# Kernel tuning notes

Measured on AMD Instinct MI355X. Metric: run time of the kernel, lower is better.

## Reference

```python
import jax, jax.numpy as jnp
import numpy as np

D_MODEL = 1024
N_HEADS = 16
HEAD_DIM = D_MODEL // N_HEADS


def setup_inputs() -> dict:
    key = jax.random.key(0)
    k1, k2, k3 = jax.random.split(key, 3)
    B, T = 2, 2048
    x = jax.random.normal(k1, (B, T, D_MODEL), dtype=jnp.float32)
    # causal lower-triangular mask; positions with mask==0 are blocked
    mask = jnp.tril(jnp.ones((T, T), dtype=jnp.int32))
    s = 1.0 / np.sqrt(D_MODEL)
    W_qkv = jax.random.normal(k2, (D_MODEL, 3 * D_MODEL), dtype=jnp.float32) * s
    W_out = jax.random.normal(k3, (D_MODEL, D_MODEL), dtype=jnp.float32) * s
    return {"x": x, "mask": mask, "W_qkv": W_qkv, "W_out": W_out}


def reference(x, mask, W_qkv, W_out):
    B, T, C = x.shape
    qkv = x @ W_qkv  # [B, T, 3C]
    q, k, v = jnp.split(qkv, 3, axis=-1)
    # [B, H, T, Dh]
    def heads(t):
        return t.reshape(B, T, N_HEADS, HEAD_DIM).transpose(0, 2, 1, 3)
    q, k, v = heads(q), heads(k), heads(v)
    scale = jnp.float32(1.0 / np.sqrt(HEAD_DIM))
    attn = jnp.einsum("bhqd,bhkd->bhqk", q, k) * scale  # [B,H,T,T]
    attn = jnp.where(mask == 0, jnp.float32(-jnp.inf), attn)
    attn = jax.nn.softmax(attn, axis=-1)
    out = jnp.einsum("bhqk,bhkd->bhqd", attn, v)  # [B,H,T,Dh]
    out = out.transpose(0, 2, 1, 3).reshape(B, T, C)
    return out @ W_out
```

## Files before the change

### kernel.cpp

```cpp
#include <hip/hip_runtime.h>
#include <hip/hip_bf16.h>

typedef __bf16 bf16;
typedef __bf16 bf16x4 __attribute__((ext_vector_type(4)));
typedef __bf16 bf16x8 __attribute__((ext_vector_type(8)));
typedef float f32x4 __attribute__((ext_vector_type(4)));
typedef float f32x16 __attribute__((ext_vector_type(16)));
typedef unsigned int uint4v __attribute__((ext_vector_type(4)));

__device__ __forceinline__ void gld_lds16(const void* g, void* l) {
  __builtin_amdgcn_global_load_lds(
      (const __attribute__((address_space(1))) void*)g,
      (__attribute__((address_space(3))) void*)l, 16, 0, 0);
}

__device__ __forceinline__ unsigned pkbf(float a, float b) {
  union { bf16 h[2]; unsigned u; } x;
  x.h[0] = (bf16)a; x.h[1] = (bf16)b;
  return x.u;
}

__global__ __launch_bounds__(256) void cvt_kernel(const float* __restrict__ src,
                                                  bf16* __restrict__ dst, int n4) {
  int i = blockIdx.x * 256 + threadIdx.x;
  if (i < n4) {
    float4 v = ((const float4*)src)[i];
    bf16x4 o = { (bf16)v.x, (bf16)v.y, (bf16)v.z, (bf16)v.w };
    ((bf16x4*)dst)[i] = o;
  }
}

__global__ __launch_bounds__(256) void transpose_cvt_kernel(const float* __restrict__ src,
                                                            bf16* __restrict__ dst,
                                                            int R, int C) {
  __shared__ float tile[32][33];
  int tx = threadIdx.x & 31, ty = threadIdx.x >> 5;
  int bx = blockIdx.x * 32, by = blockIdx.y * 32;
#pragma unroll
  for (int j = 0; j < 32; j += 8)
    tile[ty + j][tx] = src[(size_t)(by + ty + j) * C + bx + tx];
  __syncthreads();
#pragma unroll
  for (int j = 0; j < 32; j += 8)
    dst[(size_t)(bx + ty + j) * R + by + tx] = (bf16)tile[tx][ty + j];
}

template <int MODE>
__global__ __launch_bounds__(256) void gemm_kernel(
    const bf16* __restrict__ A, const bf16* __restrict__ BT,
    float* __restrict__ Cf, bf16* __restrict__ qb, bf16* __restrict__ kb,
    bf16* __restrict__ vt, int M, int N, int K) {
  __shared__ bf16 As[128 * 32];
  __shared__ bf16 Bs[128 * 32];
  const int t = threadIdx.x;
  const int w = t >> 6, l = t & 63;
  const int bm = blockIdx.y * 128, bn = blockIdx.x * 128;
  const int wr = (w >> 1) * 64, wc = (w & 1) * 64;
  const int lr = l & 15, lh = l >> 4;
  f32x4 acc[4][4] = {};

  const bf16* Ab = A + (size_t)bm * K;
  const bf16* Bb = BT + (size_t)bn * K;
  const int srow = t >> 2;
  const int scol = (t & 3) * 8;
  char* AsB = (char*)As;
  char* BsB = (char*)Bs;
  const int ldsw = w * 1024;

  for (int k0 = 0; k0 < K; k0 += 32) {
    __syncthreads();
    gld_lds16(Ab + (size_t)srow * K + k0 + scol, AsB + ldsw);
    gld_lds16(Ab + (size_t)(srow + 64) * K + k0 + scol, AsB + 4096 + ldsw);
    gld_lds16(Bb + (size_t)srow * K + k0 + scol, BsB + ldsw);
    gld_lds16(Bb + (size_t)(srow + 64) * K + k0 + scol, BsB + 4096 + ldsw);
    __syncthreads();
    bf16x8 af[4], bfr[4];
#pragma unroll
    for (int m = 0; m < 4; ++m)
      af[m] = *(const bf16x8*)(AsB + (wr + m * 16 + lr) * 64 + lh * 16);
#pragma unroll
    for (int n = 0; n < 4; ++n)
      bfr[n] = *(const bf16x8*)(BsB + (wc + n * 16 + lr) * 64 + lh * 16);
#pragma unroll
    for (int m = 0; m < 4; ++m)
#pragma unroll
      for (int n = 0; n < 4; ++n)
        acc[m][n] = __builtin_amdgcn_mfma_f32_16x16x32_bf16(af[m], bfr[n],
                                                            acc[m][n], 0, 0, 0);
  }

  const int r0 = bm + wr + (lh << 2);
  const int c0 = bn + wc + lr;
#pragma unroll
  for (int m = 0; m < 4; ++m) {
#pragma unroll
    for (int n = 0; n < 4; ++n) {
#pragma unroll
      for (int r = 0; r < 4; ++r) {
        float v = acc[m][n][r];
        int row = r0 + m * 16 + r;
        int col = c0 + n * 16;
        if (MODE == 2) {
          Cf[(size_t)row * N + col] = v;
        } else {
          int bb = row >> 11, tt = row & 2047;
          if (col < 1024) {
            int h = col >> 6, d = col & 63;
            qb[(((size_t)(bb * 16 + h)) * 2048 + tt) * 64 + d] = (bf16)v;
          } else if (col < 2048) {
            int c = col - 1024, h = c >> 6, d = c & 63;
            kb[(((size_t)(bb * 16 + h)) * 2048 + tt) * 64 + d] = (bf16)v;
          } else {
            int c = col - 2048, h = c >> 6, d = c & 63;
            vt[(((size_t)(bb * 16 + h)) * 64 + d) * 2048 + tt] = (bf16)v;
          }
        }
      }
    }
  }
}

__global__ __launch_bounds__(256) void attn_kernel(const bf16* __restrict__ qb,
                                                   const bf16* __restrict__ kb,
                                                   const bf16* __restrict__ vt,
                                                   bf16* __restrict__ ao) {
  __shared__ bf16 plds[4][32][72];
  int wid = blockIdx.y * 16 + blockIdx.x;
  int swz = (wid & 7) * 64 + (wid >> 3);
  const int bh = swz >> 4;
  const int q0 = (swz & 15) * 128;
  const int w = threadIdx.x >> 6, l = threadIdx.x & 63;
  const int qw = q0 + w * 32;
  const int lq = l & 31, hi = l >> 5;
  const bf16* Qh = qb + (size_t)bh * 2048 * 64;
  const bf16* Kh = kb + (size_t)bh * 2048 * 64;
  const bf16* Vh = vt + (size_t)bh * 64 * 2048;

  bf16x8 qf[4];
#pragma unroll
  for (int c = 0; c < 4; ++c)
    qf[c] = *(const bf16x8*)(Qh + (size_t)(qw + lq) * 64 + c * 16 + hi * 8);

  f32x16 Ot0, Ot1;
#pragma unroll
  for (int r = 0; r < 16; ++r) { Ot0[r] = 0.f; Ot1[r] = 0.f; }
  float mrun = -1e30f, srun = 0.f;
  const int lastkt = qw >> 5;

  bf16x8 kA[4], vA[4], kB[4], vB[4];
#pragma unroll
  for (int c = 0; c < 4; ++c)
    kA[c] = *(const bf16x8*)(Kh + (size_t)lq * 64 + c * 16 + hi * 8);
#pragma unroll
  for (int df = 0; df < 2; ++df)
#pragma unroll
    for (int c = 0; c < 2; ++c)
      vA[df * 2 + c] = *(const bf16x8*)(Vh + (size_t)(df * 32 + lq) * 2048 + c * 16 + hi * 8);

  auto step = [&](bf16x8 (&KC)[4], bf16x8 (&VC)[4],
                  bf16x8 (&KN)[4], bf16x8 (&VN)[4], int kt) {
    const int kv0 = kt << 5;
    const int nkv0 = (kt < lastkt) ? kv0 + 32 : kv0;
#pragma unroll
    for (int c = 0; c < 4; ++c)
      KN[c] = *(const bf16x8*)(Kh + (size_t)(nkv0 + lq) * 64 + c * 16 + hi * 8);
#pragma unroll
    for (int df = 0; df < 2; ++df)
#pragma unroll
      for (int c = 0; c < 2; ++c)
        VN[df * 2 + c] = *(const bf16x8*)(Vh + (size_t)(df * 32 + lq) * 2048 + nkv0 + c * 16 + hi * 8);

    f32x16 S;
#pragma unroll
    for (int r = 0; r < 16; ++r) S[r] = 0.f;
#pragma unroll
    for (int c = 0; c < 4; ++c)
      S = __builtin_amdgcn_mfma_f32_32x32x16_bf16(KC[c], qf[c], S, 0, 0, 0);

    if (kt == lastkt) {
#pragma unroll
      for (int r = 0; r < 16; ++r) {
        int kvl = (r & 3) + 8 * (r >> 2) + 4 * hi;
        if (kvl > lq) S[r] = -1e30f;
      }
    }

    float mx[8];
#pragma unroll
    for (int i = 0; i < 8; ++i) mx[i] = fmaxf(S[2 * i], S[2 * i + 1]);
#pragma unroll
    for (int i = 0; i < 4; ++i) mx[i] = fmaxf(mx[i], mx[i + 4]);
    mx[0] = fmaxf(mx[0], mx[2]); mx[1] = fmaxf(mx[1], mx[3]);
    float smax = fmaxf(mx[0], mx[1]);
    float vmax = fmaxf(smax, __shfl_xor(smax, 32, 64));

    float mn = mrun;
    if (!__all(vmax <= mrun + 64.0f)) {
      mn = fmaxf(mrun, vmax);
      float al = __expf((mrun - mn) * 0.125f);
      srun *= al;
#pragma unroll
      for (int r = 0; r < 16; ++r) { Ot0[r] *= al; Ot1[r] *= al; }
      mrun = mn;
    }

    const float sc = 0.125f;
    const float nb = -mn * sc;
    float ps = 0.f;
    unsigned u_[8];
#pragma unroll
    for (int i = 0; i < 8; ++i) {
      float pa = __expf(fmaf(S[2 * i], sc, nb));
      float pb = __expf(fmaf(S[2 * i + 1], sc, nb));
      ps += pa + pb;
      u_[i] = pkbf(pa, pb);
    }
    ps += __shfl_xor(ps, 32, 64);
    srun += ps;

    unsigned s_[8];
#pragma unroll
    for (int i = 0; i < 8; ++i) s_[i] = __shfl_xor(u_[i], 32, 64);

    uint4v f0 = hi ? (uint4v){s_[2], s_[3], u_[2], u_[3]}
                   : (uint4v){u_[0], u_[1], s_[0], s_[1]};
    uint4v f1 = hi ? (uint4v){s_[6], s_[7], u_[6], u_[7]}
                   : (uint4v){u_[4], u_[5], s_[4], s_[5]};
    bf16x8 pf0 = __builtin_bit_cast(bf16x8, f0);
    bf16x8 pf1 = __builtin_bit_cast(bf16x8, f1);

    Ot0 = __builtin_amdgcn_mfma_f32_32x32x16_bf16(VC[0], pf0, Ot0, 0, 0, 0);
    Ot0 = __builtin_amdgcn_mfma_f32_32x32x16_bf16(VC[1], pf1, Ot0, 0, 0, 0);
    Ot1 = __builtin_amdgcn_mfma_f32_32x32x16_bf16(VC[2], pf0, Ot1, 0, 0, 0);
    Ot1 = __builtin_amdgcn_mfma_f32_32x32x16_bf16(VC[3], pf1, Ot1, 0, 0, 0);
  };

  for (int kt = 0; kt <= lastkt; ++kt) {
    if ((kt & 1) == 0) step(kA, vA, kB, vB, kt);
    else               step(kB, vB, kA, vA, kt);
  }

  float inv = 1.0f / srun;
#pragma unroll
  for (int r = 0; r < 16; r += 2) {
    int d0 = (r & 3) + 8 * (r >> 2) + 4 * hi;
    *(unsigned*)&plds[w][lq][d0]      = pkbf(Ot0[r] * inv, Ot0[r + 1] * inv);
    *(unsigned*)&plds[w][lq][32 + d0] = pkbf(Ot1[r] * inv, Ot1[r + 1] * inv);
  }
  __syncthreads();

  const int bb = bh >> 4, h = bh & 15;
  const int q = l >> 1, dh = (l & 1) * 32;
  size_t orow = ((size_t)(bb * 2048 + qw + q)) * 1024 + h * 64 + dh;
#pragma unroll
  for (int c = 0; c < 4; ++c) {
    bf16x8 vv = *(const bf16x8*)&plds[w][q][dh + c * 8];
    *(bf16x8*)(ao + orow + c * 8) = vv;
  }
}

extern "C" void kernel_launch(void* const* d_in, const int* in_sizes, int n_in,
                              void* d_out, int out_size, void* d_ws, size_t ws_size,
                              hipStream_t stream) {
  const float* x = (const float*)d_in[0];
  const float* Wqkv = (const float*)d_in[2];
  const float* Wout = (const float*)d_in[3];
  float* out = (float*)d_out;

  char* ws = (char*)d_ws;
  bf16* xb  = (bf16*)(ws);
  bf16* wqT = (bf16*)(ws + (size_t)(8 << 20));
  bf16* woT = (bf16*)(ws + (size_t)(14 << 20));
  bf16* qb  = (bf16*)(ws + (size_t)(16 << 20));
  bf16* kb  = (bf16*)(ws + (size_t)(24 << 20));
  bf16* vt  = (bf16*)(ws + (size_t)(32 << 20));
  bf16* ao  = (bf16*)(ws + (size_t)(40 << 20));

  cvt_kernel<<<dim3(4096), dim3(256), 0, stream>>>(x, xb, 1048576);
  transpose_cvt_kernel<<<dim3(96, 32), dim3(256), 0, stream>>>(Wqkv, wqT, 1024, 3072);
  transpose_cvt_kernel<<<dim3(32, 32), dim3(256), 0, stream>>>(Wout, woT, 1024, 1024);
  gemm_kernel<1><<<dim3(24, 32), dim3(256), 0, stream>>>(xb, wqT, nullptr, qb, kb, vt,
                                                         4096, 3072, 1024);
  attn_kernel<<<dim3(16, 32), dim3(256), 0, stream>>>(qb, kb, vt, ao);
  gemm_kernel<2><<<dim3(8, 32), dim3(256), 0, stream>>>(ao, woT, out, nullptr, nullptr,
                                                        nullptr, 4096, 1024, 1024);
}
```

Baseline: 273.7 us.

## Balance causal attention work by pairing query tiles and transpose V separately

Each attention wave now handles two 32-row query tiles, j and 63-j, so every wave does the same total number of causal KV steps. The grid stays the same size but each block does twice the tiles. The QKV GEMM now writes V in row layout and a new transpose kernel builds the transposed V, replacing the strided scatter stores in the GEMM epilogue. The softmax switches to exp2f with a pre-folded log2e scale, and the barrier before the per-wave LDS readback becomes a waitcnt. This adds one kernel launch and an extra pass over V in exchange for even load across waves and more coalesced GEMM stores.

New measurement: 307.5 us. 12.3% more time.

```diff
diff --git a/kernel.cpp b/kernel.cpp
--- a/kernel.cpp
+++ b/kernel.cpp
@@ -45,11 +45,29 @@
     dst[(size_t)(bx + ty + j) * R + by + tx] = (bf16)tile[tx][ty + j];
 }
 
+__global__ __launch_bounds__(256) void transpose_v_kernel(const bf16* __restrict__ src,
+                                                          bf16* __restrict__ dst) {
+  __shared__ bf16 tile[32][34];
+  int bh = blockIdx.z;
+  int t0 = blockIdx.x * 32;
+  int d0 = blockIdx.y * 32;
+  int tx = threadIdx.x & 31, ty = threadIdx.x >> 5;
+  const bf16* s = src + (size_t)bh * 2048 * 64;
+  bf16* d = dst + (size_t)bh * 64 * 2048;
+#pragma unroll
+  for (int j = 0; j < 32; j += 8)
+    tile[ty + j][tx] = s[(size_t)(t0 + ty + j) * 64 + d0 + tx];
+  __syncthreads();
+#pragma unroll
+  for (int j = 0; j < 32; j += 8)
+    d[(size_t)(d0 + ty + j) * 2048 + t0 + tx] = tile[tx][ty + j];
+}
+
 template <int MODE>
 __global__ __launch_bounds__(256) void gemm_kernel(
     const bf16* __restrict__ A, const bf16* __restrict__ BT,
     float* __restrict__ Cf, bf16* __restrict__ qb, bf16* __restrict__ kb,
-    bf16* __restrict__ vt, int M, int N, int K) {
+    bf16* __restrict__ vb, int M, int N, int K) {
   __shared__ bf16 As[128 * 32];
   __shared__ bf16 Bs[128 * 32];
   const int t = threadIdx.x;
@@ -112,7 +130,7 @@
             kb[(((size_t)(bb * 16 + h)) * 2048 + tt) * 64 + d] = (bf16)v;
           } else {
             int c = col - 2048, h = c >> 6, d = c & 63;
-            vt[(((size_t)(bb * 16 + h)) * 64 + d) * 2048 + tt] = (bf16)v;
+            vb[(((size_t)(bb * 16 + h)) * 2048 + tt) * 64 + d] = (bf16)v;
           }
         }
       }
@@ -128,134 +146,139 @@
   int wid = blockIdx.y * 16 + blockIdx.x;
   int swz = (wid & 7) * 64 + (wid >> 3);
   const int bh = swz >> 4;
-  const int q0 = (swz & 15) * 128;
+  const int grp = swz & 15;
   const int w = threadIdx.x >> 6, l = threadIdx.x & 63;
-  const int qw = q0 + w * 32;
+  const int jj = grp * 4 + w;
   const int lq = l & 31, hi = l >> 5;
   const bf16* Qh = qb + (size_t)bh * 2048 * 64;
   const bf16* Kh = kb + (size_t)bh * 2048 * 64;
   const bf16* Vh = vt + (size_t)bh * 64 * 2048;
-
-  bf16x8 qf[4];
-#pragma unroll
-  for (int c = 0; c < 4; ++c)
-    qf[c] = *(const bf16x8*)(Qh + (size_t)(qw + lq) * 64 + c * 16 + hi * 8);
-
-  f32x16 Ot0, Ot1;
-#pragma unroll
-  for (int r = 0; r < 16; ++r) { Ot0[r] = 0.f; Ot1[r] = 0.f; }
-  float mrun = -1e30f, srun = 0.f;
-  const int lastkt = qw >> 5;
-
-  bf16x8 kA[4], vA[4], kB[4], vB[4];
-#pragma unroll
-  for (int c = 0; c < 4; ++c)
-    kA[c] = *(const bf16x8*)(Kh + (size_t)lq * 64 + c * 16 + hi * 8);
-#pragma unroll
-  for (int df = 0; df < 2; ++df)
-#pragma unroll
-    for (int c = 0; c < 2; ++c)
-      vA[df * 2 + c] = *(const bf16x8*)(Vh + (size_t)(df * 32 + lq) * 2048 + c * 16 + hi * 8);
-
-  auto step = [&](bf16x8 (&KC)[4], bf16x8 (&VC)[4],
-                  bf16x8 (&KN)[4], bf16x8 (&VN)[4], int kt) {
-    const int kv0 = kt << 5;
-    const int nkv0 = (kt < lastkt) ? kv0 + 32 : kv0;
+  const int bb = bh >> 4, h = bh & 15;
+  const float sc2 = 0.125f * 1.4426950408889634f;
+
+#pragma unroll 1
+  for (int phase = 0; phase < 2; ++phase) {
+    const int qw = (phase ? (63 - jj) : jj) * 32;
+    const int lastkt = qw >> 5;
+
+    bf16x8 qf[4];
 #pragma unroll
     for (int c = 0; c < 4; ++c)
-      KN[c] = *(const bf16x8*)(Kh + (size_t)(nkv0 + lq) * 64 + c * 16 + hi * 8);
+      qf[c] = *(const bf16x8*)(Qh + (size_t)(qw + lq) * 64 + c * 16 + hi * 8);
+
+    f32x16 Ot0, Ot1;
+#pragma unroll
+    for (int r = 0; r < 16; ++r) { Ot0[r] = 0.f; Ot1[r] = 0.f; }
+    float mrun = -1e30f, srun = 0.f;
+
+    bf16x8 kA[4], vA[4], kB[4], vB[4];
+#pragma unroll
+    for (int c = 0; c < 4; ++c)
+      kA[c] = *(const bf16x8*)(Kh + (size_t)lq * 64 + c * 16 + hi * 8);
 #pragma unroll
     for (int df = 0; df < 2; ++df)
 #pragma unroll
       for (int c = 0; c < 2; ++c)
-        VN[df * 2 + c] = *(const bf16x8*)(Vh + (size_t)(df * 32 + lq) * 2048 + nkv0 + c * 16 + hi * 8);
-
-    f32x16 S;
-#pragma unroll
-    for (int r = 0; r < 16; ++r) S[r] = 0.f;
-#pragma unroll
-    for (int c = 0; c < 4; ++c)
-      S = __builtin_amdgcn_mfma_f32_32x32x16_bf16(KC[c], qf[c], S, 0, 0, 0);
-
-    if (kt == lastkt) {
-#pragma unroll
-      for (int r = 0; r < 16; ++r) {
-        int kvl = (r & 3) + 8 * (r >> 2) + 4 * hi;
-        if (kvl > lq) S[r] = -1e30f;
+        vA[df * 2 + c] = *(const bf16x8*)(Vh + (size_t)(df * 32 + lq) * 2048 + c * 16 + hi * 8);
+
+    auto step = [&](bf16x8 (&KC)[4], bf16x8 (&VC)[4],
+                    bf16x8 (&KN)[4], bf16x8 (&VN)[4], int kt) {
+      const int kv0 = kt << 5;
+      const int nkv0 = (kt < lastkt) ? kv0 + 32 : kv0;
+#pragma unroll
+      for (int c = 0; c < 4; ++c)
+        KN[c] = *(const bf16x8*)(Kh + (size_t)(nkv0 + lq) * 64 + c * 16 + hi * 8);
+#pragma unroll
+      for (int df = 0; df < 2; ++df)
+#pragma unroll
+        for (int c = 0; c < 2; ++c)
+          VN[df * 2 + c] = *(const bf16x8*)(Vh + (size_t)(df * 32 + lq) * 2048 + nkv0 + c * 16 + hi * 8);
+
+      f32x16 S;
+#pragma unroll
+      for (int r = 0; r < 16; ++r) S[r] = 0.f;
+#pragma unroll
+      for (int c = 0; c < 4; ++c)
+        S = __builtin_amdgcn_mfma_f32_32x32x16_bf16(KC[c], qf[c], S, 0, 0, 0);
+
+      if (kt == lastkt) {
+#pragma unroll
+        for (int r = 0; r < 16; ++r) {
+          int kvl = (r & 3) + 8 * (r >> 2) + 4 * hi;
+          if (kvl > lq) S[r] = -1e30f;
+        }
       }
+
+      float mx[8];
+#pragma unroll
+      for (int i = 0; i < 8; ++i) mx[i] = fmaxf(S[2 * i], S[2 * i + 1]);
+#pragma unroll
+      for (int i = 0; i < 4; ++i) mx[i] = fmaxf(mx[i], mx[i + 4]);
+      mx[0] = fmaxf(mx[0], mx[2]); mx[1] = fmaxf(mx[1], mx[3]);
+      float smax = fmaxf(mx[0], mx[1]);
+      float vmax = fmaxf(smax, __shfl_xor(smax, 32, 64));
+
+      float mn = mrun;
+      if (!__all(vmax <= mrun + 64.0f)) {
+        mn = fmaxf(mrun, vmax);
+        float al = exp2f((mrun - mn) * sc2);
+        srun *= al;
+#pragma unroll
+        for (int r = 0; r < 16; ++r) { Ot0[r] *= al; Ot1[r] *= al; }
+        mrun = mn;
+      }
+
+      const float nb = -mn * sc2;
+      float ps = 0.f;
+      unsigned u_[8];
+#pragma unroll
+      for (int i = 0; i < 8; ++i) {
+        float pa = exp2f(fmaf(S[2 * i], sc2, nb));
+        float pb = exp2f(fmaf(S[2 * i + 1], sc2, nb));
+        ps += pa + pb;
+        u_[i] = pkbf(pa, pb);
+      }
+      ps += __shfl_xor(ps, 32, 64);
+      srun += ps;
+
+      unsigned s_[8];
+#pragma unroll
+      for (int i = 0; i < 8; ++i) s_[i] = __shfl_xor(u_[i], 32, 64);
+
+      uint4v f0 = hi ? (uint4v){s_[2], s_[3], u_[2], u_[3]}
+                     : (uint4v){u_[0], u_[1], s_[0], s_[1]};
+      uint4v f1 = hi ? (uint4v){s_[6], s_[7], u_[6], u_[7]}
+                     : (uint4v){u_[4], u_[5], s_[4], s_[5]};
+      bf16x8 pf0 = __builtin_bit_cast(bf16x8, f0);
+      bf16x8 pf1 = __builtin_bit_cast(bf16x8, f1);
+
+      Ot0 = __builtin_amdgcn_mfma_f32_32x32x16_bf16(VC[0], pf0, Ot0, 0, 0, 0);
+      Ot0 = __builtin_amdgcn_mfma_f32_32x32x16_bf16(VC[1], pf1, Ot0, 0, 0, 0);
+      Ot1 = __builtin_amdgcn_mfma_f32_32x32x16_bf16(VC[2], pf0, Ot1, 0, 0, 0);
+      Ot1 = __builtin_amdgcn_mfma_f32_32x32x16_bf16(VC[3], pf1, Ot1, 0, 0, 0);
+    };
+
+    for (int kt = 0; kt <= lastkt; ++kt) {
+      if ((kt & 1) == 0) step(kA, vA, kB, vB, kt);
+      else               step(kB, vB, kA, vA, kt);
     }
 
-    float mx[8];
-#pragma unroll
-    for (int i = 0; i < 8; ++i) mx[i] = fmaxf(S[2 * i], S[2 * i + 1]);
-#pragma unroll
-    for (int i = 0; i < 4; ++i) mx[i] = fmaxf(mx[i], mx[i + 4]);
-    mx[0] = fmaxf(mx[0], mx[2]); mx[1] = fmaxf(mx[1], mx[3]);
-    float smax = fmaxf(mx[0], mx[1]);
-    float vmax = fmaxf(smax, __shfl_xor(smax, 32, 64));
-
-    float mn = mrun;
-    if (!__all(vmax <= mrun + 64.0f)) {
-      mn = fmaxf(mrun, vmax);
-      float al = __expf((mrun - mn) * 0.125f);
-      srun *= al;
-#pragma unroll
-      for (int r = 0; r < 16; ++r) { Ot0[r] *= al; Ot1[r] *= al; }
-      mrun = mn;
+    float inv = 1.0f / srun;
+#pragma unroll
+    for (int r = 0; r < 16; r += 2) {
+      int d0 = (r & 3) + 8 * (r >> 2) + 4 * hi;
+      *(unsigned*)&plds[w][lq][d0]      = pkbf(Ot0[r] * inv, Ot0[r + 1] * inv);
+      *(unsigned*)&plds[w][lq][32 + d0] = pkbf(Ot1[r] * inv, Ot1[r + 1] * inv);
     }
-
-    const float sc = 0.125f;
-    const float nb = -mn * sc;
-    float ps = 0.f;
-    unsigned u_[8];
-#pragma unroll
-    for (int i = 0; i < 8; ++i) {
-      float pa = __expf(fmaf(S[2 * i], sc, nb));
-      float pb = __expf(fmaf(S[2 * i + 1], sc, nb));
-      ps += pa + pb;
-      u_[i] = pkbf(pa, pb);
+    __builtin_amdgcn_s_waitcnt(0);
+
+    const int q = l >> 1, dh = (l & 1) * 32;
+    size_t orow = ((size_t)(bb * 2048 + qw + q)) * 1024 + h * 64 + dh;
+#pragma unroll
+    for (int c = 0; c < 4; ++c) {
+      bf16x8 vv = *(const bf16x8*)&plds[w][q][dh + c * 8];
+      *(bf16x8*)(ao + orow + c * 8) = vv;
     }
-    ps += __shfl_xor(ps, 32, 64);
-    srun += ps;
-
-    unsigned s_[8];
-#pragma unroll
-    for (int i = 0; i < 8; ++i) s_[i] = __shfl_xor(u_[i], 32, 64);
-
-    uint4v f0 = hi ? (uint4v){s_[2], s_[3], u_[2], u_[3]}
-                   : (uint4v){u_[0], u_[1], s_[0], s_[1]};
-    uint4v f1 = hi ? (uint4v){s_[6], s_[7], u_[6], u_[7]}
-                   : (uint4v){u_[4], u_[5], s_[4], s_[5]};
-    bf16x8 pf0 = __builtin_bit_cast(bf16x8, f0);
-    bf16x8 pf1 = __builtin_bit_cast(bf16x8, f1);
-
-    Ot0 = __builtin_amdgcn_mfma_f32_32x32x16_bf16(VC[0], pf0, Ot0, 0, 0, 0);
-    Ot0 = __builtin_amdgcn_mfma_f32_32x32x16_bf16(VC[1], pf1, Ot0, 0, 0, 0);
-    Ot1 = __builtin_amdgcn_mfma_f32_32x32x16_bf16(VC[2], pf0, Ot1, 0, 0, 0);
-    Ot1 = __builtin_amdgcn_mfma_f32_32x32x16_bf16(VC[3], pf1, Ot1, 0, 0, 0);
-  };
-
-  for (int kt = 0; kt <= lastkt; ++kt) {
-    if ((kt & 1) == 0) step(kA, vA, kB, vB, kt);
-    else               step(kB, vB, kA, vA, kt);
-  }
-
-  float inv = 1.0f / srun;
-#pragma unroll
-  for (int r = 0; r < 16; r += 2) {
-    int d0 = (r & 3) + 8 * (r >> 2) + 4 * hi;
-    *(unsigned*)&plds[w][lq][d0]      = pkbf(Ot0[r] * inv, Ot0[r + 1] * inv);
-    *(unsigned*)&plds[w][lq][32 + d0] = pkbf(Ot1[r] * inv, Ot1[r + 1] * inv);
-  }
-  __syncthreads();
-
-  const int bb = bh >> 4, h = bh & 15;
-  const int q = l >> 1, dh = (l & 1) * 32;
-  size_t orow = ((size_t)(bb * 2048 + qw + q)) * 1024 + h * 64 + dh;
-#pragma unroll
-  for (int c = 0; c < 4; ++c) {
-    bf16x8 vv = *(const bf16x8*)&plds[w][q][dh + c * 8];
-    *(bf16x8*)(ao + orow + c * 8) = vv;
   }
 }
 
@@ -275,12 +298,14 @@
   bf16* kb  = (bf16*)(ws + (size_t)(24 << 20));
   bf16* vt  = (bf16*)(ws + (size_t)(32 << 20));
   bf16* ao  = (bf16*)(ws + (size_t)(40 << 20));
+  bf16* vb  = (bf16*)(ws + (size_t)(48 << 20));
 
   cvt_kernel<<<dim3(4096), dim3(256), 0, stream>>>(x, xb, 1048576);
   transpose_cvt_kernel<<<dim3(96, 32), dim3(256), 0, stream>>>(Wqkv, wqT, 1024, 3072);
   transpose_cvt_kernel<<<dim3(32, 32), dim3(256), 0, stream>>>(Wout, woT, 1024, 1024);
-  gemm_kernel<1><<<dim3(24, 32), dim3(256), 0, stream>>>(xb, wqT, nullptr, qb, kb, vt,
+  gemm_kernel<1><<<dim3(24, 32), dim3(256), 0, stream>>>(xb, wqT, nullptr, qb, kb, vb,
                                                          4096, 3072, 1024);
+  transpose_v_kernel<<<dim3(64, 2, 32), dim3(256), 0, stream>>>(vb, vt);
   attn_kernel<<<dim3(16, 32), dim3(256), 0, stream>>>(qb, kb, vt, ao);
   gemm_kernel<2><<<dim3(8, 32), dim3(256), 0, stream>>>(ao, woT, out, nullptr, nullptr,
                                                         nullptr, 4096, 1024, 1024);
```
